# Performance work log

Hardware: AMD Instinct MI355X
Metric: run time of the kernel (lower is better)

Reference implementation:

```python
import jax, jax.numpy as jnp
import numpy as np

B, S, V, F, H = 256, 512, 50000, 64, 256


def setup_inputs() -> dict:
    key = jax.random.key(0)
    ks = jax.random.split(key, 12)
    s_in = 1.0 / np.sqrt(F)
    s_hid = 1.0 / np.sqrt(H)
    return {
        "batch": jax.random.randint(ks[0], (B, S), 0, V),
        "features": jax.random.normal(ks[1], (V, F), jnp.float32),
        "W_ih0": jax.random.normal(ks[2], (H, F), jnp.float32) * s_in,
        "W_hh0": jax.random.normal(ks[3], (H, H), jnp.float32) * s_hid,
        "b_ih0": jax.random.normal(ks[4], (H,), jnp.float32) * s_hid,
        "b_hh0": jax.random.normal(ks[5], (H,), jnp.float32) * s_hid,
        "W_ih1": jax.random.normal(ks[6], (H, H), jnp.float32) * s_hid,
        "W_hh1": jax.random.normal(ks[7], (H, H), jnp.float32) * s_hid,
        "b_ih1": jax.random.normal(ks[8], (H,), jnp.float32) * s_hid,
        "b_hh1": jax.random.normal(ks[9], (H,), jnp.float32) * s_hid,
        "W_out": jax.random.normal(ks[10], (V, H), jnp.float32) * s_hid,
        "b_out": jax.random.normal(ks[11], (V,), jnp.float32) * s_hid,
    }


def _rnn_layer(x, W_ih, W_hh, b_ih, b_hh):
    # x: [B, S, Din] -> [B, S, H]; torch tanh RNN: h_t = tanh(x_t W_ih^T + b_ih + h_{t-1} W_hh^T + b_hh)
    xW = jnp.einsum('bsd,hd->bsh', x, W_ih) + (b_ih + b_hh)  # precompute input projection
    h0 = jnp.zeros((x.shape[0], W_hh.shape[0]), x.dtype)

    def step(h, xt):
        h = jnp.tanh(xt + h @ W_hh.T)
        return h, h

    _, ys = jax.lax.scan(step, h0, jnp.swapaxes(xW, 0, 1))  # scan over time
    return jnp.swapaxes(ys, 0, 1)


def reference(batch, features, W_ih0, W_hh0, b_ih0, b_hh0,
              W_ih1, W_hh1, b_ih1, b_hh1, W_out, b_out):
    # vectorized replacement of the nested per-token gather loop
    full_representation = features[batch]            # [B, S, F]
    h = _rnn_layer(full_representation, W_ih0, W_hh0, b_ih0, b_hh0)
    h = _rnn_layer(h, W_ih1, W_hh1, b_ih1, b_hh1)    # [B, S, H]
    return h[:, -1, :] @ W_out.T + b_out             # [B, V]
```

## Files before the change

kernel.cpp:

```cpp
#include <hip/hip_runtime.h>

#define B_ 256
#define S_ 512
#define V_ 50000
#define F_ 64
#define H_ 256

typedef _Float16 f16;
typedef _Float16 f16x2 __attribute__((ext_vector_type(2)));
typedef _Float16 f16x4 __attribute__((ext_vector_type(4)));
typedef _Float16 f16x8 __attribute__((ext_vector_type(8)));
typedef float f32x4 __attribute__((ext_vector_type(4)));

__device__ __forceinline__ f16x8 cvt8(const float4 a, const float4 b) {
    f16x8 v;
    v[0] = (f16)a.x; v[1] = (f16)a.y; v[2] = (f16)a.z; v[3] = (f16)a.w;
    v[4] = (f16)b.x; v[5] = (f16)b.y; v[6] = (f16)b.z; v[7] = (f16)b.w;
    return v;
}

__device__ __forceinline__ float fast_tanh(float x) {
    float e = __expf(2.f * x);
    float r = __builtin_amdgcn_rcpf(e + 1.f);
    return __builtin_fmaf(-2.f, r, 1.f);
}

__global__ __launch_bounds__(512) void k_vocab_proj(
    const float* __restrict__ feat, const float* __restrict__ Wih,
    const float* __restrict__ bi, const float* __restrict__ bh,
    f16* __restrict__ T)
{
    __shared__ char Wl[256 * 128];
    __shared__ char Xl[16 * 128];
    const int tid = threadIdx.x;
    {
        const int n = tid >> 1, k0 = (tid & 1) << 5;
#pragma unroll
        for (int k = k0; k < k0 + 32; k += 8) {
            float4 a = *(const float4*)(Wih + n * F_ + k);
            float4 b = *(const float4*)(Wih + n * F_ + k + 4);
            *(f16x8*)(Wl + n * 128 + (((k >> 3) ^ (n & 7)) << 4)) = cvt8(a, b);
        }
    }
    const int v0 = blockIdx.x * 16;
    {
        const int m = tid >> 5, k = (tid & 31) << 1;
        float2 a = *(const float2*)(feat + (v0 + m) * F_ + k);
        f16x2 v; v[0] = (f16)a.x; v[1] = (f16)a.y;
        *(f16x2*)(Xl + m * 128 + ((((k >> 3) ^ (m & 7)) << 4) | ((k & 7) << 1))) = v;
    }
    __syncthreads();
    const int lane = tid & 63, w = tid >> 6;
    const int q = lane & 15, g = lane >> 4;
#pragma unroll
    for (int nt = 0; nt < 2; ++nt) {
        const int n0 = w * 32 + nt * 16;
        const int nrow = n0 + q;
        float4 b1 = *(const float4*)(bi + n0 + g * 4);
        float4 b2 = *(const float4*)(bh + n0 + g * 4);
        f32x4 acc = {b1.x + b2.x, b1.y + b2.y, b1.z + b2.z, b1.w + b2.w};
#pragma unroll
        for (int kb = 0; kb < 2; ++kb) {
            f16x8 a = *(const f16x8*)(Wl + nrow * 128 + (((kb * 4 + g) ^ (nrow & 7)) << 4));
            f16x8 b = *(const f16x8*)(Xl + q * 128 + (((kb * 4 + g) ^ (q & 7)) << 4));
            acc = __builtin_amdgcn_mfma_f32_16x16x32_f16(a, b, acc, 0, 0, 0);
        }
        f16x4 o; o[0] = (f16)acc[0]; o[1] = (f16)acc[1]; o[2] = (f16)acc[2]; o[3] = (f16)acc[3];
        *(f16x4*)(T + (size_t)(v0 + q) * H_ + n0 + g * 4) = o;
    }
}

__global__ __launch_bounds__(256) void k_gather(
    const int* __restrict__ idx, const f16* __restrict__ T, f16* __restrict__ xw)
{
    const size_t stride = (size_t)gridDim.x * blockDim.x;
    const size_t total = (size_t)B_ * S_ * 32;
    for (size_t ci = (size_t)blockIdx.x * blockDim.x + threadIdx.x; ci < total; ci += stride) {
        const size_t r = ci >> 5;
        const int c = (int)(ci & 31);
        const size_t row = (size_t)idx[r];
        *(f16x8*)(xw + r * H_ + c * 8) = *(const f16x8*)(T + row * H_ + c * 8);
    }
}

template <bool WRITE_ALL>
__device__ __forceinline__ void rnn_step(
    const int t, const f16* xw, f16* hout, const f16x8 (&wf)[2][8],
    f16x4 (&xv)[2],
    const char* rbuf, char* wbuf,
    const int brow, const int ncol, const int g, const int hrow, const int hswz)
{
    f32x4 acc[2], accB[2];
#pragma unroll
    for (int tt = 0; tt < 2; ++tt) {
        acc[tt][0] = (float)xv[tt][0]; acc[tt][1] = (float)xv[tt][1];
        acc[tt][2] = (float)xv[tt][2]; acc[tt][3] = (float)xv[tt][3];
        accB[tt][0] = 0.f; accB[tt][1] = 0.f; accB[tt][2] = 0.f; accB[tt][3] = 0.f;
    }
    if (t + 2 < S_) {
        const size_t rb2 = ((size_t)brow * S_ + t + 2) * H_;
#pragma unroll
        for (int tt = 0; tt < 2; ++tt)
            xv[tt] = *(const f16x4*)(xw + rb2 + ncol + tt * 16 + g * 4);
    }
#pragma unroll
    for (int kb = 0; kb < 4; ++kb) {
        f16x8 bf0 = *(const f16x8*)(rbuf + hrow + ((kb * 64 + g * 16) ^ hswz));
        f16x8 bf1 = *(const f16x8*)(rbuf + hrow + (((kb + 4) * 64 + g * 16) ^ hswz));
#pragma unroll
        for (int tt = 0; tt < 2; ++tt) {
            acc[tt]  = __builtin_amdgcn_mfma_f32_16x16x32_f16(wf[tt][kb],     bf0, acc[tt],  0, 0, 0);
            accB[tt] = __builtin_amdgcn_mfma_f32_16x16x32_f16(wf[tt][kb + 4], bf1, accB[tt], 0, 0, 0);
        }
    }
    f16x4 hv[2];
#pragma unroll
    for (int tt = 0; tt < 2; ++tt)
#pragma unroll
        for (int r = 0; r < 4; ++r)
            hv[tt][r] = (f16)fast_tanh(acc[tt][r] + accB[tt][r]);
#pragma unroll
    for (int tt = 0; tt < 2; ++tt) {
        const int nd = ncol + tt * 16 + g * 4;
        *(f16x4*)(wbuf + hrow + ((nd * 2) ^ hswz)) = hv[tt];
    }
    if (WRITE_ALL) {
#pragma unroll
        for (int tt = 0; tt < 2; ++tt)
            *(f16x4*)(hout + ((size_t)brow * S_ + t) * H_ + ncol + tt * 16 + g * 4) = hv[tt];
    } else if (t == S_ - 1) {
#pragma unroll
        for (int tt = 0; tt < 2; ++tt)
            *(f16x4*)(hout + (size_t)brow * H_ + ncol + tt * 16 + g * 4) = hv[tt];
    }
    asm volatile("s_waitcnt lgkmcnt(0)\n\ts_barrier" ::: "memory");
}

template <bool WRITE_ALL>
__global__ __launch_bounds__(512, 1) void k_recur(
    const f16* xw, const float* __restrict__ Whh, f16* hout)
{
    __shared__ char hbuf[2][16 * 512];
    const int tid = threadIdx.x, lane = tid & 63, w = tid >> 6;
    const int q = lane & 15, g = lane >> 4;
    const int brow = (blockIdx.x << 4) + q;
    const int ncol = w * 32;

    f16x8 wf[2][8];
#pragma unroll
    for (int tt = 0; tt < 2; ++tt) {
        const int n = ncol + tt * 16 + q;
#pragma unroll
        for (int kb = 0; kb < 8; ++kb) {
            float4 a = *(const float4*)(Whh + n * H_ + kb * 32 + g * 8);
            float4 b = *(const float4*)(Whh + n * H_ + kb * 32 + g * 8 + 4);
            wf[tt][kb] = cvt8(a, b);
        }
    }
    {
        f32x4 z = {0.f, 0.f, 0.f, 0.f};
        *(f32x4*)(hbuf[1] + tid * 16) = z;
    }
    const int hswz = (q & 7) << 4;
    const int hrow = q * 512;

    f16x4 xa[2], xb[2];
    {
        const size_t r0 = (size_t)brow * S_ * H_;
#pragma unroll
        for (int tt = 0; tt < 2; ++tt) {
            xa[tt] = *(const f16x4*)(xw + r0 + ncol + tt * 16 + g * 4);
            xb[tt] = *(const f16x4*)(xw + r0 + H_ + ncol + tt * 16 + g * 4);
        }
    }
    __syncthreads();

    for (int t = 0; t < S_; t += 2) {
        rnn_step<WRITE_ALL>(t,     xw, hout, wf, xa, hbuf[1], hbuf[0],
                            brow, ncol, g, hrow, hswz);
        rnn_step<WRITE_ALL>(t + 1, xw, hout, wf, xb, hbuf[0], hbuf[1],
                            brow, ncol, g, hrow, hswz);
    }
}

__global__ __launch_bounds__(512) void k_proj1(
    f16* __restrict__ h0, const float* __restrict__ Wih,
    const float* __restrict__ bi, const float* __restrict__ bh)
{
    __shared__ char Wl[256 * 512];
    __shared__ char Al[32 * 512];
    const int tid = threadIdx.x;
    {
        const int n = tid >> 1, k0 = (tid & 1) << 7;
#pragma unroll
        for (int k = k0; k < k0 + 128; k += 8) {
            float4 a = *(const float4*)(Wih + n * H_ + k);
            float4 b = *(const float4*)(Wih + n * H_ + k + 4);
            *(f16x8*)(Wl + n * 512 + (((k >> 3) ^ (n & 7)) << 4)) = cvt8(a, b);
        }
    }
    const int lane = tid & 63, w = tid >> 6;
    const int q = lane & 15, g = lane >> 4;
    for (int rb = blockIdx.x; rb < (B_ * S_) / 32; rb += gridDim.x) {
        const size_t r0 = (size_t)rb * 32;
        __syncthreads();
        {
            const int m = tid >> 4, blk0 = (tid & 15) << 1;
#pragma unroll
            for (int i = 0; i < 2; ++i) {
                const int blk = blk0 + i;
                f16x8 v = *(const f16x8*)(h0 + (r0 + m) * H_ + blk * 8);
                *(f16x8*)(Al + m * 512 + ((blk ^ (m & 7)) << 4)) = v;
            }
        }
        __syncthreads();
        f32x4 acc[2][2];
#pragma unroll
        for (int nt = 0; nt < 2; ++nt) {
            const int nb = w * 32 + nt * 16 + g * 4;
            float4 b1 = *(const float4*)(bi + nb);
            float4 b2 = *(const float4*)(bh + nb);
#pragma unroll
            for (int mt = 0; mt < 2; ++mt) {
                acc[nt][mt][0] = b1.x + b2.x; acc[nt][mt][1] = b1.y + b2.y;
                acc[nt][mt][2] = b1.z + b2.z; acc[nt][mt][3] = b1.w + b2.w;
            }
        }
#pragma unroll
        for (int kb = 0; kb < 8; ++kb) {
            f16x8 af[2], bf[2];
#pragma unroll
            for (int nt = 0; nt < 2; ++nt) {
                const int nrow = w * 32 + nt * 16 + q;
                af[nt] = *(const f16x8*)(Wl + nrow * 512 + (((kb * 4 + g) ^ (nrow & 7)) << 4));
            }
#pragma unroll
            for (int mt = 0; mt < 2; ++mt) {
                const int mrow = mt * 16 + q;
                bf[mt] = *(const f16x8*)(Al + mrow * 512 + (((kb * 4 + g) ^ (mrow & 7)) << 4));
            }
#pragma unroll
            for (int nt = 0; nt < 2; ++nt)
#pragma unroll
                for (int mt = 0; mt < 2; ++mt)
                    acc[nt][mt] = __builtin_amdgcn_mfma_f32_16x16x32_f16(af[nt], bf[mt], acc[nt][mt], 0, 0, 0);
        }
#pragma unroll
        for (int nt = 0; nt < 2; ++nt) {
            const int nb = w * 32 + nt * 16 + g * 4;
#pragma unroll
            for (int mt = 0; mt < 2; ++mt) {
                f16x4 o;
                o[0] = (f16)acc[nt][mt][0]; o[1] = (f16)acc[nt][mt][1];
                o[2] = (f16)acc[nt][mt][2]; o[3] = (f16)acc[nt][mt][3];
                *(f16x4*)(h0 + (r0 + mt * 16 + q) * H_ + nb) = o;
            }
        }
    }
}

__global__ __launch_bounds__(512) void k_out(
    const f16* __restrict__ h1, const float* __restrict__ Wout,
    const float* __restrict__ bout, float* __restrict__ out)
{
    __shared__ char Hl[256 * 512];
    const int tid = threadIdx.x;
    {
        const int m = tid >> 1, half = tid & 1;
#pragma unroll
        for (int i = 0; i < 16; ++i) {
            const int blk = half * 16 + i;
            f16x8 v = *(const f16x8*)(h1 + m * H_ + blk * 8);
            *(f16x8*)(Hl + m * 512 + ((blk ^ (m & 7)) << 4)) = v;
        }
    }
    __syncthreads();
    const int lane = tid & 63, w = tid >> 6;
    const int q = lane & 15, g = lane >> 4;
    const int v0 = blockIdx.x * 80;
    f32x4 acc[5][2];
#pragma unroll
    for (int vt = 0; vt < 5; ++vt) {
        float4 bo = *(const float4*)(bout + v0 + vt * 16 + g * 4);
#pragma unroll
        for (int bt = 0; bt < 2; ++bt) {
            acc[vt][bt][0] = bo.x; acc[vt][bt][1] = bo.y;
            acc[vt][bt][2] = bo.z; acc[vt][bt][3] = bo.w;
        }
    }
#pragma unroll
    for (int kb = 0; kb < 8; ++kb) {
        f16x8 bf[2];
#pragma unroll
        for (int bt = 0; bt < 2; ++bt) {
            const int mrow = (w * 2 + bt) * 16 + q;
            bf[bt] = *(const f16x8*)(Hl + mrow * 512 + (((kb * 4 + g) ^ (mrow & 7)) << 4));
        }
#pragma unroll
        for (int vt = 0; vt < 5; ++vt) {
            const size_t vrow = v0 + vt * 16 + q;
            float4 a = *(const float4*)(Wout + vrow * H_ + kb * 32 + g * 8);
            float4 b = *(const float4*)(Wout + vrow * H_ + kb * 32 + g * 8 + 4);
            f16x8 af = cvt8(a, b);
#pragma unroll
            for (int bt = 0; bt < 2; ++bt)
                acc[vt][bt] = __builtin_amdgcn_mfma_f32_16x16x32_f16(af, bf[bt], acc[vt][bt], 0, 0, 0);
        }
    }
#pragma unroll
    for (int vt = 0; vt < 5; ++vt)
#pragma unroll
        for (int bt = 0; bt < 2; ++bt) {
            const int b = (w * 2 + bt) * 16 + q;
            const int v = v0 + vt * 16 + g * 4;
            float4 o = {acc[vt][bt][0], acc[vt][bt][1], acc[vt][bt][2], acc[vt][bt][3]};
            *(float4*)(out + (size_t)b * V_ + v) = o;
        }
}

extern "C" void kernel_launch(void* const* d_in, const int* in_sizes, int n_in,
                              void* d_out, int out_size, void* d_ws, size_t ws_size,
                              hipStream_t stream) {
    (void)in_sizes; (void)n_in; (void)out_size; (void)ws_size;
    const int*   batch = (const int*)  d_in[0];
    const float* feat  = (const float*)d_in[1];
    const float* Wih0  = (const float*)d_in[2];
    const float* Whh0  = (const float*)d_in[3];
    const float* bih0  = (const float*)d_in[4];
    const float* bhh0  = (const float*)d_in[5];
    const float* Wih1  = (const float*)d_in[6];
    const float* Whh1  = (const float*)d_in[7];
    const float* bih1  = (const float*)d_in[8];
    const float* bhh1  = (const float*)d_in[9];
    const float* Wout  = (const float*)d_in[10];
    const float* bout  = (const float*)d_in[11];
    float* out = (float*)d_out;

    f16* T  = (f16*)d_out;
    f16* h0 = (f16*)d_ws;
    f16* h1 = (f16*)((char*)d_ws + (size_t)B_ * S_ * H_ * 2);

    k_vocab_proj<<<dim3(V_ / 16), dim3(512), 0, stream>>>(feat, Wih0, bih0, bhh0, T);
    k_gather<<<dim3(2048), dim3(256), 0, stream>>>(batch, T, h0);
    k_recur<true><<<dim3(16), dim3(512), 0, stream>>>(h0, Whh0, h0);
    k_proj1<<<dim3(512), dim3(512), 0, stream>>>(h0, Wih1, bih1, bhh1);
    k_recur<false><<<dim3(16), dim3(512), 0, stream>>>(h0, Whh1, h1);
    k_out<<<dim3(625), dim3(512), 0, stream>>>(h1, Wout, bout, out);
}
```

Before: 948.5 us.

## Fuse gather, both RNN layers and layer-1 projection into one wavefront-pipelined kernel

Replaces the gather, layer-0 recurrence, layer-1 input projection and layer-1 recurrence kernels with a single kernel. Layer 1 runs one timestep behind layer 0 within the same step, and the vocab-table rows are gathered directly by index. This removes the full B*S*H intermediate writes and reads and halves the number of serial barrier-separated steps, since the two recurrences overlap. The cost is three weight matrices held in registers (launch bounds 512,2 may cause spills), and each step now carries a longer chain of 48 MFMAs plus two tanh passes.

```diff
diff --git a/kernel.cpp b/kernel.cpp
--- a/kernel.cpp
+++ b/kernel.cpp
@@ -70,193 +70,220 @@
     }
 }
 
-__global__ __launch_bounds__(256) void k_gather(
-    const int* __restrict__ idx, const f16* __restrict__ T, f16* __restrict__ xw)
+__global__ __launch_bounds__(512, 2) void k_fused(
+    const f16* __restrict__ T, const int* __restrict__ idx,
+    const float* __restrict__ Whh0, const float* __restrict__ Wih1,
+    const float* __restrict__ bih1, const float* __restrict__ bhh1,
+    const float* __restrict__ Whh1, f16* __restrict__ h1out)
 {
-    const size_t stride = (size_t)gridDim.x * blockDim.x;
-    const size_t total = (size_t)B_ * S_ * 32;
-    for (size_t ci = (size_t)blockIdx.x * blockDim.x + threadIdx.x; ci < total; ci += stride) {
-        const size_t r = ci >> 5;
-        const int c = (int)(ci & 31);
-        const size_t row = (size_t)idx[r];
-        *(f16x8*)(xw + r * H_ + c * 8) = *(const f16x8*)(T + row * H_ + c * 8);
-    }
-}
-
-template <bool WRITE_ALL>
-__device__ __forceinline__ void rnn_step(
-    const int t, const f16* xw, f16* hout, const f16x8 (&wf)[2][8],
-    f16x4 (&xv)[2],
-    const char* rbuf, char* wbuf,
-    const int brow, const int ncol, const int g, const int hrow, const int hswz)
-{
-    f32x4 acc[2], accB[2];
-#pragma unroll
-    for (int tt = 0; tt < 2; ++tt) {
-        acc[tt][0] = (float)xv[tt][0]; acc[tt][1] = (float)xv[tt][1];
-        acc[tt][2] = (float)xv[tt][2]; acc[tt][3] = (float)xv[tt][3];
-        accB[tt][0] = 0.f; accB[tt][1] = 0.f; accB[tt][2] = 0.f; accB[tt][3] = 0.f;
-    }
-    if (t + 2 < S_) {
-        const size_t rb2 = ((size_t)brow * S_ + t + 2) * H_;
-#pragma unroll
-        for (int tt = 0; tt < 2; ++tt)
-            xv[tt] = *(const f16x4*)(xw + rb2 + ncol + tt * 16 + g * 4);
-    }
-#pragma unroll
-    for (int kb = 0; kb < 4; ++kb) {
-        f16x8 bf0 = *(const f16x8*)(rbuf + hrow + ((kb * 64 + g * 16) ^ hswz));
-        f16x8 bf1 = *(const f16x8*)(rbuf + hrow + (((kb + 4) * 64 + g * 16) ^ hswz));
-#pragma unroll
-        for (int tt = 0; tt < 2; ++tt) {
-            acc[tt]  = __builtin_amdgcn_mfma_f32_16x16x32_f16(wf[tt][kb],     bf0, acc[tt],  0, 0, 0);
-            accB[tt] = __builtin_amdgcn_mfma_f32_16x16x32_f16(wf[tt][kb + 4], bf1, accB[tt], 0, 0, 0);
-        }
-    }
-    f16x4 hv[2];
-#pragma unroll
-    for (int tt = 0; tt < 2; ++tt)
-#pragma unroll
-        for (int r = 0; r < 4; ++r)
-            hv[tt][r] = (f16)fast_tanh(acc[tt][r] + accB[tt][r]);
-#pragma unroll
-    for (int tt = 0; tt < 2; ++tt) {
-        const int nd = ncol + tt * 16 + g * 4;
-        *(f16x4*)(wbuf + hrow + ((nd * 2) ^ hswz)) = hv[tt];
-    }
-    if (WRITE_ALL) {
-#pragma unroll
-        for (int tt = 0; tt < 2; ++tt)
-            *(f16x4*)(hout + ((size_t)brow * S_ + t) * H_ + ncol + tt * 16 + g * 4) = hv[tt];
-    } else if (t == S_ - 1) {
-#pragma unroll
-        for (int tt = 0; tt < 2; ++tt)
-            *(f16x4*)(hout + (size_t)brow * H_ + ncol + tt * 16 + g * 4) = hv[tt];
-    }
-    asm volatile("s_waitcnt lgkmcnt(0)\n\ts_barrier" ::: "memory");
-}
-
-template <bool WRITE_ALL>
-__global__ __launch_bounds__(512, 1) void k_recur(
-    const f16* xw, const float* __restrict__ Whh, f16* hout)
-{
-    __shared__ char hbuf[2][16 * 512];
+    __shared__ char h0b[2][8192];
+    __shared__ char h1b[2][8192];
     const int tid = threadIdx.x, lane = tid & 63, w = tid >> 6;
     const int q = lane & 15, g = lane >> 4;
     const int brow = (blockIdx.x << 4) + q;
     const int ncol = w * 32;
-
-    f16x8 wf[2][8];
+    const int hswz = (q & 7) << 4;
+    const int hrow = q * 512;
+
+    f16x8 wA[2][8], wP[2][8], wC[2][8];
 #pragma unroll
     for (int tt = 0; tt < 2; ++tt) {
         const int n = ncol + tt * 16 + q;
 #pragma unroll
         for (int kb = 0; kb < 8; ++kb) {
-            float4 a = *(const float4*)(Whh + n * H_ + kb * 32 + g * 8);
-            float4 b = *(const float4*)(Whh + n * H_ + kb * 32 + g * 8 + 4);
-            wf[tt][kb] = cvt8(a, b);
-        }
+            const int o = n * H_ + kb * 32 + g * 8;
+            wA[tt][kb] = cvt8(*(const float4*)(Whh0 + o), *(const float4*)(Whh0 + o + 4));
+            wP[tt][kb] = cvt8(*(const float4*)(Wih1 + o), *(const float4*)(Wih1 + o + 4));
+            wC[tt][kb] = cvt8(*(const float4*)(Whh1 + o), *(const float4*)(Whh1 + o + 4));
+        }
+    }
+    f32x4 bs1[2];
+#pragma unroll
+    for (int tt = 0; tt < 2; ++tt) {
+        const int n = ncol + tt * 16 + g * 4;
+        float4 x = *(const float4*)(bih1 + n);
+        float4 y = *(const float4*)(bhh1 + n);
+        bs1[tt][0] = x.x + y.x; bs1[tt][1] = x.y + y.y;
+        bs1[tt][2] = x.z + y.z; bs1[tt][3] = x.w + y.w;
     }
     {
         f32x4 z = {0.f, 0.f, 0.f, 0.f};
-        *(f32x4*)(hbuf[1] + tid * 16) = z;
-    }
-    const int hswz = (q & 7) << 4;
-    const int hrow = q * 512;
-
+        *(f32x4*)(h0b[1] + tid * 16) = z;
+        *(f32x4*)(h1b[1] + tid * 16) = z;
+    }
+    const int* idxr = idx + brow * S_;
     f16x4 xa[2], xb[2];
     {
-        const size_t r0 = (size_t)brow * S_ * H_;
-#pragma unroll
-        for (int tt = 0; tt < 2; ++tt) {
-            xa[tt] = *(const f16x4*)(xw + r0 + ncol + tt * 16 + g * 4);
-            xb[tt] = *(const f16x4*)(xw + r0 + H_ + ncol + tt * 16 + g * 4);
-        }
-    }
+        const size_t r0 = (size_t)idxr[0] * H_, r1 = (size_t)idxr[1] * H_;
+#pragma unroll
+        for (int tt = 0; tt < 2; ++tt) {
+            xa[tt] = *(const f16x4*)(T + r0 + ncol + tt * 16 + g * 4);
+            xb[tt] = *(const f16x4*)(T + r1 + ncol + tt * 16 + g * 4);
+        }
+    }
+    int idA = idxr[2], idB = idxr[3];
     __syncthreads();
 
-    for (int t = 0; t < S_; t += 2) {
-        rnn_step<WRITE_ALL>(t,     xw, hout, wf, xa, hbuf[1], hbuf[0],
-                            brow, ncol, g, hrow, hswz);
-        rnn_step<WRITE_ALL>(t + 1, xw, hout, wf, xb, hbuf[0], hbuf[1],
-                            brow, ncol, g, hrow, hswz);
-    }
-}
-
-__global__ __launch_bounds__(512) void k_proj1(
-    f16* __restrict__ h0, const float* __restrict__ Wih,
-    const float* __restrict__ bi, const float* __restrict__ bh)
-{
-    __shared__ char Wl[256 * 512];
-    __shared__ char Al[32 * 512];
-    const int tid = threadIdx.x;
-    {
-        const int n = tid >> 1, k0 = (tid & 1) << 7;
-#pragma unroll
-        for (int k = k0; k < k0 + 128; k += 8) {
-            float4 a = *(const float4*)(Wih + n * H_ + k);
-            float4 b = *(const float4*)(Wih + n * H_ + k + 4);
-            *(f16x8*)(Wl + n * 512 + (((k >> 3) ^ (n & 7)) << 4)) = cvt8(a, b);
-        }
-    }
-    const int lane = tid & 63, w = tid >> 6;
-    const int q = lane & 15, g = lane >> 4;
-    for (int rb = blockIdx.x; rb < (B_ * S_) / 32; rb += gridDim.x) {
-        const size_t r0 = (size_t)rb * 32;
-        __syncthreads();
+#define FR(buf, kb) (*(const f16x8*)((buf) + hrow + (((kb) * 64 + g * 16) ^ hswz)))
+#define STEP_BAR() do { \
+        asm volatile("s_waitcnt lgkmcnt(0)" ::: "memory"); \
+        __builtin_amdgcn_s_barrier(); \
+        __builtin_amdgcn_sched_barrier(0); \
+    } while (0)
+
+#define BODY(XV, ID, RD0, WR0, RD1, WR1, T_) do {                               \
+        f32x4 a0[2], p[2];                                                      \
+        _Pragma("unroll")                                                       \
+        for (int tt = 0; tt < 2; ++tt) {                                        \
+            a0[tt][0] = (float)XV[tt][0]; a0[tt][1] = (float)XV[tt][1];         \
+            a0[tt][2] = (float)XV[tt][2]; a0[tt][3] = (float)XV[tt][3];         \
+            p[tt] = bs1[tt];                                                    \
+        }                                                                       \
+        {       \
+            const size_t rr = (size_t)ID * H_;                                  \
+            _Pragma("unroll")                                                   \
+            for (int tt = 0; tt < 2; ++tt)                                      \
+                XV[tt] = *(const f16x4*)(T + rr + ncol + tt * 16 + g * 4);      \
+            const int t4 = (T_ + 4 < S_) ? T_ + 4 : S_ - 1;                     \
+            ID = idxr[t4];                                                      \
+        }                                                                       \
+        _Pragma("unroll")                                                       \
+        for (int kb = 0; kb < 8; ++kb) {                                        \
+            f16x8 bf = FR(RD0, kb);                                             \
+            a0[0] = __builtin_amdgcn_mfma_f32_16x16x32_f16(wA[0][kb], bf, a0[0], 0, 0, 0); \
+            a0[1] = __builtin_amdgcn_mfma_f32_16x16x32_f16(wA[1][kb], bf, a0[1], 0, 0, 0); \
+            p[0]  = __builtin_amdgcn_mfma_f32_16x16x32_f16(wP[0][kb], bf, p[0], 0, 0, 0);  \
+            p[1]  = __builtin_amdgcn_mfma_f32_16x16x32_f16(wP[1][kb], bf, p[1], 0, 0, 0);  \
+        }                                                                       \
+        _Pragma("unroll")                                                       \
+        for (int tt = 0; tt < 2; ++tt) {                       \
+            f16x4 hv;                                                           \
+            _Pragma("unroll")                                                   \
+            for (int r = 0; r < 4; ++r) hv[r] = (f16)fast_tanh(a0[tt][r]);      \
+            const int nd = ncol + tt * 16 + g * 4;                              \
+            *(f16x4*)(WR0 + hrow + ((nd * 2) ^ hswz)) = hv;                     \
+        }                                                                       \
+        _Pragma("unroll")                                                       \
+        for (int kb = 0; kb < 8; ++kb) {                                        \
+            f16x8 cf = FR(RD1, kb);                                             \
+            p[0] = __builtin_amdgcn_mfma_f32_16x16x32_f16(wC[0][kb], cf, p[0], 0, 0, 0); \
+            p[1] = __builtin_amdgcn_mfma_f32_16x16x32_f16(wC[1][kb], cf, p[1], 0, 0, 0); \
+        }                                                                       \
+        _Pragma("unroll")                                                       \
+        for (int tt = 0; tt < 2; ++tt) {                  \
+            f16x4 hv;                                                           \
+            _Pragma("unroll")                                                   \
+            for (int r = 0; r < 4; ++r) hv[r] = (f16)fast_tanh(p[tt][r]);       \
+            const int nd = ncol + tt * 16 + g * 4;                              \
+            *(f16x4*)(WR1 + hrow + ((nd * 2) ^ hswz)) = hv;                     \
+        }                                                                       \
+        STEP_BAR();                                                             \
+    } while (0)
+
+    {
+        f32x4 a0[2];
+#pragma unroll
+        for (int tt = 0; tt < 2; ++tt) {
+            a0[tt][0] = (float)xa[tt][0]; a0[tt][1] = (float)xa[tt][1];
+            a0[tt][2] = (float)xa[tt][2]; a0[tt][3] = (float)xa[tt][3];
+        }
         {
-            const int m = tid >> 4, blk0 = (tid & 15) << 1;
-#pragma unroll
-            for (int i = 0; i < 2; ++i) {
-                const int blk = blk0 + i;
-                f16x8 v = *(const f16x8*)(h0 + (r0 + m) * H_ + blk * 8);
-                *(f16x8*)(Al + m * 512 + ((blk ^ (m & 7)) << 4)) = v;
-            }
-        }
-        __syncthreads();
-        f32x4 acc[2][2];
-#pragma unroll
-        for (int nt = 0; nt < 2; ++nt) {
-            const int nb = w * 32 + nt * 16 + g * 4;
-            float4 b1 = *(const float4*)(bi + nb);
-            float4 b2 = *(const float4*)(bh + nb);
-#pragma unroll
-            for (int mt = 0; mt < 2; ++mt) {
-                acc[nt][mt][0] = b1.x + b2.x; acc[nt][mt][1] = b1.y + b2.y;
-                acc[nt][mt][2] = b1.z + b2.z; acc[nt][mt][3] = b1.w + b2.w;
-            }
-        }
-#pragma unroll
-        for (int kb = 0; kb < 8; ++kb) {
-            f16x8 af[2], bf[2];
-#pragma unroll
-            for (int nt = 0; nt < 2; ++nt) {
-                const int nrow = w * 32 + nt * 16 + q;
-                af[nt] = *(const f16x8*)(Wl + nrow * 512 + (((kb * 4 + g) ^ (nrow & 7)) << 4));
-            }
-#pragma unroll
-            for (int mt = 0; mt < 2; ++mt) {
-                const int mrow = mt * 16 + q;
-                bf[mt] = *(const f16x8*)(Al + mrow * 512 + (((kb * 4 + g) ^ (mrow & 7)) << 4));
-            }
-#pragma unroll
-            for (int nt = 0; nt < 2; ++nt)
-#pragma unroll
-                for (int mt = 0; mt < 2; ++mt)
-                    acc[nt][mt] = __builtin_amdgcn_mfma_f32_16x16x32_f16(af[nt], bf[mt], acc[nt][mt], 0, 0, 0);
-        }
-#pragma unroll
-        for (int nt = 0; nt < 2; ++nt) {
-            const int nb = w * 32 + nt * 16 + g * 4;
-#pragma unroll
-            for (int mt = 0; mt < 2; ++mt) {
-                f16x4 o;
-                o[0] = (f16)acc[nt][mt][0]; o[1] = (f16)acc[nt][mt][1];
-                o[2] = (f16)acc[nt][mt][2]; o[3] = (f16)acc[nt][mt][3];
-                *(f16x4*)(h0 + (r0 + mt * 16 + q) * H_ + nb) = o;
-            }
-        }
-    }
+            const size_t rr = (size_t)idA * H_;
+#pragma unroll
+            for (int tt = 0; tt < 2; ++tt)
+                xa[tt] = *(const f16x4*)(T + rr + ncol + tt * 16 + g * 4);
+            idA = idxr[4];
+        }
+#pragma unroll
+        for (int kb = 0; kb < 8; ++kb) {
+            f16x8 bf = FR(h0b[1], kb);
+            a0[0] = __builtin_amdgcn_mfma_f32_16x16x32_f16(wA[0][kb], bf, a0[0], 0, 0, 0);
+            a0[1] = __builtin_amdgcn_mfma_f32_16x16x32_f16(wA[1][kb], bf, a0[1], 0, 0, 0);
+        }
+#pragma unroll
+        for (int tt = 0; tt < 2; ++tt) {
+            f16x4 hv;
+#pragma unroll
+            for (int r = 0; r < 4; ++r) hv[r] = (f16)fast_tanh(a0[tt][r]);
+            const int nd = ncol + tt * 16 + g * 4;
+            *(f16x4*)(h0b[0] + hrow + ((nd * 2) ^ hswz)) = hv;
+        }
+        STEP_BAR();
+    }
+
+    for (int t = 1; t < S_ - 1; t += 2) {
+        BODY(xb, idB, h0b[0], h0b[1], h1b[1], h1b[0], t);
+        BODY(xa, idA, h0b[1], h0b[0], h1b[0], h1b[1], t + 1);
+    }
+
+    {
+        f32x4 a0[2], p[2];
+#pragma unroll
+        for (int tt = 0; tt < 2; ++tt) {
+            a0[tt][0] = (float)xb[tt][0]; a0[tt][1] = (float)xb[tt][1];
+            a0[tt][2] = (float)xb[tt][2]; a0[tt][3] = (float)xb[tt][3];
+            p[tt] = bs1[tt];
+        }
+#pragma unroll
+        for (int kb = 0; kb < 8; ++kb) {
+            f16x8 bf = FR(h0b[0], kb);
+            a0[0] = __builtin_amdgcn_mfma_f32_16x16x32_f16(wA[0][kb], bf, a0[0], 0, 0, 0);
+            a0[1] = __builtin_amdgcn_mfma_f32_16x16x32_f16(wA[1][kb], bf, a0[1], 0, 0, 0);
+            p[0]  = __builtin_amdgcn_mfma_f32_16x16x32_f16(wP[0][kb], bf, p[0], 0, 0, 0);
+            p[1]  = __builtin_amdgcn_mfma_f32_16x16x32_f16(wP[1][kb], bf, p[1], 0, 0, 0);
+        }
+#pragma unroll
+        for (int tt = 0; tt < 2; ++tt) {
+            f16x4 hv;
+#pragma unroll
+            for (int r = 0; r < 4; ++r) hv[r] = (f16)fast_tanh(a0[tt][r]);
+            const int nd = ncol + tt * 16 + g * 4;
+            *(f16x4*)(h0b[1] + hrow + ((nd * 2) ^ hswz)) = hv;
+        }
+#pragma unroll
+        for (int kb = 0; kb < 8; ++kb) {
+            f16x8 cf = FR(h1b[1], kb);
+            p[0] = __builtin_amdgcn_mfma_f32_16x16x32_f16(wC[0][kb], cf, p[0], 0, 0, 0);
+            p[1] = __builtin_amdgcn_mfma_f32_16x16x32_f16(wC[1][kb], cf, p[1], 0, 0, 0);
+        }
+#pragma unroll
+        for (int tt = 0; tt < 2; ++tt) {
+            f16x4 hv;
+#pragma unroll
+            for (int r = 0; r < 4; ++r) hv[r] = (f16)fast_tanh(p[tt][r]);
+            const int nd = ncol + tt * 16 + g * 4;
+            *(f16x4*)(h1b[0] + hrow + ((nd * 2) ^ hswz)) = hv;
+        }
+        STEP_BAR();
+    }
+
+    {
+        f32x4 p[2];
+#pragma unroll
+        for (int tt = 0; tt < 2; ++tt) p[tt] = bs1[tt];
+#pragma unroll
+        for (int kb = 0; kb < 8; ++kb) {
+            f16x8 bf = FR(h0b[1], kb);
+            p[0] = __builtin_amdgcn_mfma_f32_16x16x32_f16(wP[0][kb], bf, p[0], 0, 0, 0);
+            p[1] = __builtin_amdgcn_mfma_f32_16x16x32_f16(wP[1][kb], bf, p[1], 0, 0, 0);
+        }
+#pragma unroll
+        for (int kb = 0; kb < 8; ++kb) {
+            f16x8 cf = FR(h1b[0], kb);
+            p[0] = __builtin_amdgcn_mfma_f32_16x16x32_f16(wC[0][kb], cf, p[0], 0, 0, 0);
+            p[1] = __builtin_amdgcn_mfma_f32_16x16x32_f16(wC[1][kb], cf, p[1], 0, 0, 0);
+        }
+#pragma unroll
+        for (int tt = 0; tt < 2; ++tt) {
+            f16x4 hv;
+#pragma unroll
+            for (int r = 0; r < 4; ++r) hv[r] = (f16)fast_tanh(p[tt][r]);
+            *(f16x4*)(h1out + (size_t)brow * H_ + ncol + tt * 16 + g * 4) = hv;
+        }
+    }
+#undef BODY
+#undef STEP_BAR
+#undef FR
 }
 
 __global__ __launch_bounds__(512) void k_out(
@@ -337,13 +364,9 @@
     float* out = (float*)d_out;
 
     f16* T  = (f16*)d_out;
-    f16* h0 = (f16*)d_ws;
-    f16* h1 = (f16*)((char*)d_ws + (size_t)B_ * S_ * H_ * 2);
+    f16* h1 = (f16*)d_ws;
 
     k_vocab_proj<<<dim3(V_ / 16), dim3(512), 0, stream>>>(feat, Wih0, bih0, bhh0, T);
-    k_gather<<<dim3(2048), dim3(256), 0, stream>>>(batch, T, h0);
-    k_recur<true><<<dim3(16), dim3(512), 0, stream>>>(h0, Whh0, h0);
-    k_proj1<<<dim3(512), dim3(512), 0, stream>>>(h0, Wih1, bih1, bhh1);
-    k_recur<false><<<dim3(16), dim3(512), 0, stream>>>(h0, Whh1, h1);
+    k_fused<<<dim3(16), dim3(512), 0, stream>>>(T, batch, Whh0, Wih1, bih1, bhh1, Whh1, h1);
     k_out<<<dim3(625), dim3(512), 0, stream>>>(h1, Wout, bout, out);
 }
```

After: 1.273 ms. +34.2%, slower.
